# Kernel tuning notes

Measured on AMD Instinct MI355X. Metric: run time of the kernel, lower is better.

## Reference

```python
import jax, jax.numpy as jnp
import numpy as np

B, L, D = 4, 2048, 2048
NH, HD, K = 32, 64, 16
LR = 1.0
EPS = 1e-6


def ln_fwd(x, gamma, beta):
    mu = x.mean(-1, keepdims=True)
    var = jnp.var(x, axis=-1, keepdims=True)
    x_hat = (x - mu) / jnp.sqrt(var + EPS)
    return gamma * x_hat + beta


def ln_fused_l2_bwd(x, target, gamma, beta):
    # grad of 0.5*||LN(x)-target||^2 wrt x (matches LayerNormFunction.backward
    # with grad_output = LN(x) - target)
    d = x.shape[-1]
    mu = x.mean(-1, keepdims=True)
    var = jnp.var(x, axis=-1, keepdims=True)
    std = jnp.sqrt(var + EPS)
    x_hat = (x - mu) / std
    y = gamma * x_hat + beta
    g = (y - target) * gamma
    return (d * g - g.sum(-1, keepdims=True) - x_hat * (g * x_hat).sum(-1, keepdims=True)) / (d * std)


def setup_inputs() -> dict:
    key = jax.random.key(0)
    ks = jax.random.split(key, 12)
    s = 0.02
    return {
        "hidden_states": jax.random.normal(ks[0], (B, L, D), jnp.float32),
        "Wq": jax.random.normal(ks[1], (D, D), jnp.float32) * s,
        "Wk": jax.random.normal(ks[2], (D, D), jnp.float32) * s,
        "Wv": jax.random.normal(ks[3], (D, D), jnp.float32) * s,
        "Wo": jax.random.normal(ks[4], (D, D), jnp.float32) * s,
        "linear_weight": jax.random.normal(ks[5], (NH, 1, D), jnp.float32) * s,
        "linear_bias": jnp.zeros((NH, 1), jnp.float32),
        "ln_weight": jnp.ones((NH, HD), jnp.float32),
        "ln_bias": jnp.zeros((NH, HD), jnp.float32),
        "W1_init": jax.random.normal(ks[6], (NH, HD, HD), jnp.float32) * s,
        "b1_init": jnp.zeros((NH, 1, HD), jnp.float32),
    }


def reference(hidden_states, Wq, Wk, Wv, Wo, linear_weight, linear_bias,
              ln_weight, ln_bias, W1_init, b1_init):
    Bq, Lq, Dq = hidden_states.shape
    n_chunk = Lq // K

    def split(x):  # [B,L,D] -> [B,NH,n_chunk,K,HD]
        return x.reshape(Bq, n_chunk, K, NH, HD).transpose(0, 3, 1, 2, 4)

    XC = split(hidden_states @ Wq.T)
    XB = split(hidden_states @ Wk.T)
    XA = split(hidden_states @ Wv.T)

    # inner-loop learning-rate coefficient: [B,NH,n_chunk,K,1]
    X = hidden_states.reshape(Bq, n_chunk, K, Dq)
    ilr = jnp.einsum('bnkd,hd->bhnk', X, linear_weight[:, 0, :]) + linear_bias[:, 0][None, :, None, None]
    ilr_gated = jax.nn.sigmoid(ilr)[..., None]
    token_idx = 1.0 / jnp.arange(1, K + 1, dtype=hidden_states.dtype)
    coeff = (LR * token_idx).reshape(1, 1, 1, K, 1) * ilr_gated / HD

    ln_w = ln_weight.reshape(1, NH, 1, HD)
    ln_b = ln_bias.reshape(1, NH, 1, HD)
    mask = jnp.tril(jnp.ones((K, K), hidden_states.dtype))

    W1 = jnp.broadcast_to(W1_init[None], (Bq, NH, HD, HD))
    b1 = jnp.broadcast_to(b1_init[None], (Bq, NH, 1, HD))

    def step(carry, inp):
        W1, b1 = carry
        xc, xb, xa, co = inp  # [B,NH,K,HD], co: [B,NH,K,1]
        Z1 = xb @ W1 + b1
        grad = ln_fused_l2_bwd(Z1, xa - xb, ln_w, ln_b)  # [B,NH,K,HD]
        Attn = mask * jnp.einsum('bhkf,bhjf->bhkj', xc, xb)
        E = mask * co.transpose(0, 1, 3, 2)  # E[i,j] = coeff_j * (j<=i)
        b1_bar = b1 - E @ grad
        Z1_bar = xc @ W1 - (Attn * E) @ grad + b1_bar
        W1_new = W1 - jnp.einsum('bhkf,bhkg->bhfg', co * xb, grad)
        b1_new = b1 - (co * grad).sum(-2, keepdims=True)
        out = xc + ln_fwd(Z1_bar, ln_w, ln_b)
        return (W1_new, b1_new), out

    xs = (XC.transpose(2, 0, 1, 3, 4), XB.transpose(2, 0, 1, 3, 4),
          XA.transpose(2, 0, 1, 3, 4), coeff.transpose(2, 0, 1, 3, 4))
    (_, _), outs = jax.lax.scan(step, (W1, b1), xs)
    # outs: [n_chunk,B,NH,K,HD] -> [B,L,D]
    XCW = outs.transpose(1, 0, 3, 2, 4).reshape(Bq, Lq, Dq)
    return XCW @ Wo.T
```

## Files before the change

kernel.cpp:

```cpp
#include <hip/hip_runtime.h>


typedef __attribute__((ext_vector_type(4))) float float4v;
typedef __attribute__((ext_vector_type(2))) float float2v;
typedef __attribute__((ext_vector_type(8))) __bf16 bf16x8;
typedef __attribute__((ext_vector_type(4))) short short4v;
typedef __attribute__((ext_vector_type(4))) unsigned int uint4v;
typedef __attribute__((ext_vector_type(2))) unsigned int uint2v;

__device__ __forceinline__ unsigned short f2bf(float f) {
  unsigned int u = __builtin_bit_cast(unsigned int, f);
  u += 0x7FFFu + ((u >> 16) & 1u);
  return (unsigned short)(u >> 16);
}
__device__ __forceinline__ float bf2f(unsigned short s) {
  unsigned int u = ((unsigned int)s) << 16;
  return __builtin_bit_cast(float, u);
}
__device__ __forceinline__ void lds_load16(const void* g, void* l) {
  __builtin_amdgcn_global_load_lds((const __attribute__((address_space(1))) void*)g,
                                   (__attribute__((address_space(3))) void*)l, 16, 0, 0);
}

__device__ __forceinline__ void store_out(float* p, float v) { *p = v; }
__device__ __forceinline__ void store_out(unsigned short* p, float v) { *p = f2bf(v); }

template <int CTRL>
__device__ __forceinline__ float dppmov(float x) {
  return __builtin_bit_cast(
      float, __builtin_amdgcn_update_dpp(0, __builtin_bit_cast(int, x), CTRL, 0xF, 0xF, true));
}
__device__ __forceinline__ float red16(float x) {
  x += dppmov<0xB1>(x);
  x += dppmov<0x4E>(x);
  x += dppmov<0x124>(x);
  x += dppmov<0x128>(x);
  return x;
}
__device__ __forceinline__ unsigned int cvtpk_bf16(float lo, float hi) {
  unsigned int r;
  asm("v_cvt_pk_bf16_f32 %0, %1, %2" : "=v"(r) : "v"(lo), "v"(hi));
  return r;
}
__device__ __forceinline__ void bar_sync() {
  asm volatile("s_waitcnt lgkmcnt(0)" ::: "memory");
  __builtin_amdgcn_s_barrier();
  asm volatile("" ::: "memory");
}
__device__ __forceinline__ void vm_bar() {
  asm volatile("s_waitcnt vmcnt(0)" ::: "memory");
  __builtin_amdgcn_s_barrier();
  asm volatile("" ::: "memory");
}

template <typename OUT>
__global__ __launch_bounds__(256) void gemm_bt(
    const unsigned short* __restrict__ A, const unsigned short* __restrict__ B,
    OUT* __restrict__ C, int M, int N, int K) {
  __shared__ unsigned short sA[2][128 * 32];
  __shared__ unsigned short sB[2][128 * 32];
  const int tid = threadIdx.x;
  const int wave = tid >> 6;
  const int lane = tid & 63;
  const int quad = lane >> 4;
  const int l15 = lane & 15;
  const int wm = (wave >> 1) * 64;
  const int wn = (wave & 1) * 64;
  const int bm = blockIdx.y * 128;
  const int bn = blockIdx.x * 128;

  float4v acc[4][4];
#pragma unroll
  for (int i = 0; i < 4; ++i)
#pragma unroll
    for (int j = 0; j < 4; ++j) acc[i][j] = (float4v){0.f, 0.f, 0.f, 0.f};

  const int srow = tid >> 2;
  const int scol = (tid & 3) * 8;
  const unsigned short* aptr = A + (size_t)(bm + srow) * K + scol;
  const unsigned short* bptr = B + (size_t)(bn + srow) * K + scol;
  const size_t astep = (size_t)64 * K;
  const int woff = wave * 512;

  lds_load16(aptr, &sA[0][woff]);
  lds_load16(aptr + astep, &sA[0][2048 + woff]);
  lds_load16(bptr, &sB[0][woff]);
  lds_load16(bptr + astep, &sB[0][2048 + woff]);
  vm_bar();

  int cur = 0;
  for (int kt = 0; kt < K; kt += 32) {
    if (kt + 32 < K) {
      const int nxt = cur ^ 1;
      lds_load16(aptr + kt + 32, &sA[nxt][woff]);
      lds_load16(aptr + kt + 32 + astep, &sA[nxt][2048 + woff]);
      lds_load16(bptr + kt + 32, &sB[nxt][woff]);
      lds_load16(bptr + kt + 32 + astep, &sB[nxt][2048 + woff]);
    }
    bf16x8 af[4], bf[4];
#pragma unroll
    for (int i = 0; i < 4; ++i)
      af[i] = *(const bf16x8*)&sA[cur][(wm + i * 16 + l15) * 32 + quad * 8];
#pragma unroll
    for (int j = 0; j < 4; ++j)
      bf[j] = *(const bf16x8*)&sB[cur][(wn + j * 16 + l15) * 32 + quad * 8];
#pragma unroll
    for (int i = 0; i < 4; ++i)
#pragma unroll
      for (int j = 0; j < 4; ++j)
        acc[i][j] = __builtin_amdgcn_mfma_f32_16x16x32_bf16(af[i], bf[j], acc[i][j], 0, 0, 0);
    vm_bar();
    cur ^= 1;
  }

#pragma unroll
  for (int i = 0; i < 4; ++i) {
    const int row0 = bm + wm + i * 16 + quad * 4;
#pragma unroll
    for (int j = 0; j < 4; ++j) {
      const int col = bn + wn + j * 16 + l15;
#pragma unroll
      for (int r = 0; r < 4; ++r)
        store_out(&C[(size_t)(row0 + r) * N + col], acc[i][j][r]);
    }
  }
}

__global__ __launch_bounds__(256) void f32_to_bf16_k(const float* __restrict__ s,
                                                     unsigned short* __restrict__ d, int n) {
  const int i = (blockIdx.x * 256 + threadIdx.x) * 8;
  if (i >= n) return;
  const float4v a = *(const float4v*)(s + i);
  const float4v b = *(const float4v*)(s + i + 4);
  uint4v o;
  o[0] = (unsigned int)f2bf(a[0]) | ((unsigned int)f2bf(a[1]) << 16);
  o[1] = (unsigned int)f2bf(a[2]) | ((unsigned int)f2bf(a[3]) << 16);
  o[2] = (unsigned int)f2bf(b[0]) | ((unsigned int)f2bf(b[1]) << 16);
  o[3] = (unsigned int)f2bf(b[2]) | ((unsigned int)f2bf(b[3]) << 16);
  *(uint4v*)(d + i) = o;
}

__global__ __launch_bounds__(256) void coeff_k(const unsigned short* __restrict__ ilr,
                                               const float* __restrict__ lb,
                                               float* __restrict__ coeff) {
  const int gid = blockIdx.x * 256 + threadIdx.x;
  const int row = gid >> 5;
  const int h = gid & 31;
  const float v = bf2f(ilr[row * 128 + h]) + lb[h];
  const float sig = 1.0f / (1.0f + __expf(-v));
  const int b = row >> 11;
  const int pos = row & 2047;
  const int cc = pos >> 4;
  const int k = pos & 15;
  coeff[((((size_t)b * 32 + h) * 128 + cc) << 4) + k] = sig / (64.0f * (float)(k + 1));
}

__global__ __launch_bounds__(256, 1) void ttt_scan(
    const unsigned short* __restrict__ XC, const unsigned short* __restrict__ XB,
    const unsigned short* __restrict__ XA, const float* __restrict__ coeff,
    const float* __restrict__ lnw, const float* __restrict__ lnb,
    const float* __restrict__ W1i, const float* __restrict__ b1i,
    unsigned short* __restrict__ XCW) {
  const int b = blockIdx.x >> 5;
  const int h = blockIdx.x & 31;
  const int tid = threadIdx.x;
  const int wave = tid >> 6;
  const int lane = tid & 63;
  const int quad = lane >> 4;
  const int l15 = lane & 15;

  constexpr int LDW = 88;
  __shared__ __attribute__((aligned(16))) unsigned short sXC[2][16 * LDW];
  __shared__ __attribute__((aligned(16))) unsigned short sXB[2][16 * LDW];
  __shared__ __attribute__((aligned(16))) unsigned short sXA[2][16 * LDW];
  __shared__ __attribute__((aligned(16))) unsigned short sW1[64 * LDW];
  __shared__ __attribute__((aligned(16))) float sRed[3][16][8];

  const int fcol = wave * 16 + l15;
  const float gam = lnw[h * 64 + fcol];
  const float bet = lnb[h * 64 + fcol];

  float4v W1r[4];
#pragma unroll
  for (int mt = 0; mt < 4; ++mt) {
    float4v v;
#pragma unroll
    for (int r = 0; r < 4; ++r)
      v[r] = W1i[(size_t)h * 4096 + (size_t)(mt * 16 + quad * 4 + r) * 64 + fcol];
    W1r[mt] = v;
  }
  float b1v = b1i[h * 64 + fcol];

#pragma unroll
  for (int mt = 0; mt < 4; ++mt) {
    uint2v p;
    p[0] = cvtpk_bf16(W1r[mt][0], W1r[mt][1]);
    p[1] = cvtpk_bf16(W1r[mt][2], W1r[mt][3]);
    *(uint2v*)&sW1[(size_t)fcol * LDW + mt * 16 + quad * 4] = p;
  }

  const int u = tid & 127;
  const int grow = u >> 3;
  const int gcol = (u & 7) * 8;
  const size_t hdoff = (size_t)h * 64;
  const size_t browoff = (size_t)b * 2048;
  const float* cobase = coeff + (((size_t)b * 32 + h) * 128) * 16;
  const float inv64 = 1.0f / 64.0f;
  const float4v zero4 = {0.f, 0.f, 0.f, 0.f};

  uint4v pA = {0, 0, 0, 0}, pB = {0, 0, 0, 0};
  float4v pcof;
  {
    const size_t goff = (browoff + (size_t)grow) * 2048 + hdoff + gcol;
    if (tid < 128) {
      pA = *(const uint4v*)(XC + goff);
      pB = *(const uint4v*)(XA + goff);
    } else {
      pA = *(const uint4v*)(XB + goff);
    }
    pcof = *(const float4v*)(cobase + quad * 4);
  }

  for (int c = 0; c < 128; ++c) {
    const int buf = c & 1;
    if (tid < 128) {
      *(uint4v*)&sXC[buf][grow * LDW + gcol] = pA;
      *(uint4v*)&sXA[buf][grow * LDW + gcol] = pB;
    } else {
      *(uint4v*)&sXB[buf][grow * LDW + gcol] = pA;
    }
    const float4v cof = pcof;
    bar_sync();

    {
      const int cn = (c < 127) ? c + 1 : 127;
      const size_t goff = (browoff + (size_t)(cn * 16 + grow)) * 2048 + hdoff + gcol;
      if (tid < 128) {
        pA = *(const uint4v*)(XC + goff);
        pB = *(const uint4v*)(XA + goff);
      } else {
        pA = *(const uint4v*)(XB + goff);
      }
      pcof = *(const float4v*)(cobase + (size_t)cn * 16 + quad * 4);
    }

    bf16x8 xbf[2], xcf[2], w1f[2];
#pragma unroll
    for (int hh = 0; hh < 2; ++hh) {
      xbf[hh] = *(const bf16x8*)&sXB[buf][l15 * LDW + hh * 32 + quad * 8];
      xcf[hh] = *(const bf16x8*)&sXC[buf][l15 * LDW + hh * 32 + quad * 8];
      w1f[hh] = *(const bf16x8*)&sW1[(size_t)fcol * LDW + hh * 32 + quad * 8];
    }

    float4v z = __builtin_amdgcn_mfma_f32_16x16x32_bf16(xbf[0], w1f[0], zero4, 0, 0, 0);
    z = __builtin_amdgcn_mfma_f32_16x16x32_bf16(xbf[1], w1f[1], z, 0, 0, 0);
#pragma unroll
    for (int r = 0; r < 4; ++r) z[r] += b1v;

    float s1p[4], s2p[4];
#pragma unroll
    for (int r = 0; r < 4; ++r) {
      s1p[r] = red16(z[r]);
      s2p[r] = red16(z[r] * z[r]);
    }
    if (l15 == 0) {
#pragma unroll
      for (int r = 0; r < 4; ++r)
        *(float2v*)&sRed[0][quad * 4 + r][wave * 2] = (float2v){s1p[r], s2p[r]};
    }

    float4v at = __builtin_amdgcn_mfma_f32_16x16x32_bf16(xbf[0], xcf[0], zero4, 0, 0, 0);
    at = __builtin_amdgcn_mfma_f32_16x16x32_bf16(xbf[1], xcf[1], at, 0, 0, 0);

    bar_sync();

    float mu[4], rstd[4];
#pragma unroll
    for (int r = 0; r < 4; ++r) {
      const float4v v0 = *(const float4v*)&sRed[0][quad * 4 + r][0];
      const float4v v1 = *(const float4v*)&sRed[0][quad * 4 + r][4];
      const float s1 = v0[0] + v0[2] + v1[0] + v1[2];
      const float s2 = v0[1] + v0[3] + v1[1] + v1[3];
      mu[r] = s1 * inv64;
      rstd[r] = rsqrtf(s2 * inv64 - mu[r] * mu[r] + 1e-6f);
    }
    float xh[4], gg[4];
#pragma unroll
    for (int r = 0; r < 4; ++r) {
      xh[r] = (z[r] - mu[r]) * rstd[r];
      const int toff = (quad * 4 + r) * LDW + fcol;
      const float tgt = bf2f(sXA[buf][toff]) - bf2f(sXB[buf][toff]);
      gg[r] = (gam * xh[r] + bet - tgt) * gam;
    }
    float sgp[4], sgxp[4];
#pragma unroll
    for (int r = 0; r < 4; ++r) {
      sgp[r] = red16(gg[r]);
      sgxp[r] = red16(gg[r] * xh[r]);
    }
    if (l15 == 0) {
#pragma unroll
      for (int r = 0; r < 4; ++r)
        *(float2v*)&sRed[1][quad * 4 + r][wave * 2] = (float2v){sgp[r], sgxp[r]};
    }

    short4v caf[4];
#pragma unroll
    for (int mt = 0; mt < 4; ++mt)
#pragma unroll
      for (int jj = 0; jj < 4; ++jj)
        caf[mt][jj] =
            (short)f2bf(-cof[jj] * bf2f(sXB[buf][(quad * 4 + jj) * LDW + mt * 16 + l15]));
    short4v m1f;
#pragma unroll
    for (int jj = 0; jj < 4; ++jj) {
      const int k = quad * 4 + jj;
      const float e = (k <= l15) ? cof[jj] : 0.0f;
      m1f[jj] = (short)f2bf(-(at[jj] + 1.0f) * e);
    }

    bar_sync();

    float grad[4];
    short4v gradb;
#pragma unroll
    for (int r = 0; r < 4; ++r) {
      const float4v v0 = *(const float4v*)&sRed[1][quad * 4 + r][0];
      const float4v v1 = *(const float4v*)&sRed[1][quad * 4 + r][4];
      const float sg = v0[0] + v0[2] + v1[0] + v1[2];
      const float sgx = v0[1] + v0[3] + v1[1] + v1[3];
      grad[r] = (64.0f * gg[r] - sg - xh[r] * sgx) * (rstd[r] * inv64);
      gradb[r] = (short)f2bf(grad[r]);
    }

    float4v zb = __builtin_amdgcn_mfma_f32_16x16x32_bf16(xcf[0], w1f[0], zero4, 0, 0, 0);
    zb = __builtin_amdgcn_mfma_f32_16x16x32_bf16(xcf[1], w1f[1], zb, 0, 0, 0);
    zb = __builtin_amdgcn_mfma_f32_16x16x16bf16_1k(m1f, gradb, zb, 0, 0, 0);
#pragma unroll
    for (int r = 0; r < 4; ++r) zb[r] += b1v;

#pragma unroll
    for (int r = 0; r < 4; ++r) {
      s1p[r] = red16(zb[r]);
      s2p[r] = red16(zb[r] * zb[r]);
    }
    if (l15 == 0) {
#pragma unroll
      for (int r = 0; r < 4; ++r)
        *(float2v*)&sRed[2][quad * 4 + r][wave * 2] = (float2v){s1p[r], s2p[r]};
    }

    {
      float pb = cof[0] * grad[0] + cof[1] * grad[1] + cof[2] * grad[2] + cof[3] * grad[3];
      pb += __shfl_xor(pb, 16);
      pb += __shfl_xor(pb, 32);
      b1v -= pb;
    }
#pragma unroll
    for (int mt = 0; mt < 4; ++mt)
      W1r[mt] = __builtin_amdgcn_mfma_f32_16x16x16bf16_1k(caf[mt], gradb, W1r[mt], 0, 0, 0);

    bar_sync();

#pragma unroll
    for (int r = 0; r < 4; ++r) {
      const float4v v0 = *(const float4v*)&sRed[2][quad * 4 + r][0];
      const float4v v1 = *(const float4v*)&sRed[2][quad * 4 + r][4];
      const float s1 = v0[0] + v0[2] + v1[0] + v1[2];
      const float s2 = v0[1] + v0[3] + v1[1] + v1[3];
      const float mu2 = s1 * inv64;
      const float rstd2 = rsqrtf(s2 * inv64 - mu2 * mu2 + 1e-6f);
      const float xhat = (zb[r] - mu2) * rstd2;
      const float y = gam * xhat + bet;
      const float o = bf2f(sXC[buf][(quad * 4 + r) * LDW + fcol]) + y;
      XCW[(browoff + (size_t)(c * 16 + quad * 4 + r)) * 2048 + hdoff + fcol] = f2bf(o);
    }

#pragma unroll
    for (int mt = 0; mt < 4; ++mt) {
      uint2v p;
      p[0] = cvtpk_bf16(W1r[mt][0], W1r[mt][1]);
      p[1] = cvtpk_bf16(W1r[mt][2], W1r[mt][3]);
      *(uint2v*)&sW1[(size_t)fcol * LDW + mt * 16 + quad * 4] = p;
    }
  }
}

extern "C" void kernel_launch(void* const* d_in, const int* in_sizes, int n_in,
                              void* d_out, int out_size, void* d_ws, size_t ws_size,
                              hipStream_t stream) {
  const float* hs = (const float*)d_in[0];
  const float* Wq = (const float*)d_in[1];
  const float* Wk = (const float*)d_in[2];
  const float* Wv = (const float*)d_in[3];
  const float* Wo = (const float*)d_in[4];
  const float* lw = (const float*)d_in[5];
  const float* lb = (const float*)d_in[6];
  const float* lnw = (const float*)d_in[7];
  const float* lnb = (const float*)d_in[8];
  const float* W1i = (const float*)d_in[9];
  const float* b1i = (const float*)d_in[10];
  float* out = (float*)d_out;
  char* ws = (char*)d_ws;

  unsigned short* hsb = (unsigned short*)(ws);
  unsigned short* wqb = (unsigned short*)(ws + 33554432);
  unsigned short* wkb = (unsigned short*)(ws + 41943040);
  unsigned short* wvb = (unsigned short*)(ws + 50331648);
  unsigned short* wob = (unsigned short*)(ws + 58720256);
  unsigned short* lwb = (unsigned short*)(ws + 67108864);
  unsigned short* XCb = (unsigned short*)(ws + 67633152);
  unsigned short* XBb = (unsigned short*)(ws + 101187584);
  unsigned short* XAb = (unsigned short*)(ws + 134742016);
  unsigned short* ilrb = (unsigned short*)(ws + 168296448);
  float* coeff = (float*)(ws + 170393600);

  f32_to_bf16_k<<<8192, 256, 0, stream>>>(hs, hsb, 16777216);
  f32_to_bf16_k<<<2048, 256, 0, stream>>>(Wq, wqb, 4194304);
  f32_to_bf16_k<<<2048, 256, 0, stream>>>(Wk, wkb, 4194304);
  f32_to_bf16_k<<<2048, 256, 0, stream>>>(Wv, wvb, 4194304);
  f32_to_bf16_k<<<2048, 256, 0, stream>>>(Wo, wob, 4194304);
  hipMemsetAsync(lwb, 0, 524288, stream);
  f32_to_bf16_k<<<32, 256, 0, stream>>>(lw, lwb, 65536);

  dim3 blk(256);
  dim3 gbig(16, 64);
  gemm_bt<unsigned short><<<gbig, blk, 0, stream>>>(hsb, wqb, XCb, 8192, 2048, 2048);
  gemm_bt<unsigned short><<<gbig, blk, 0, stream>>>(hsb, wkb, XBb, 8192, 2048, 2048);
  gemm_bt<unsigned short><<<gbig, blk, 0, stream>>>(hsb, wvb, XAb, 8192, 2048, 2048);
  gemm_bt<unsigned short><<<dim3(1, 64), blk, 0, stream>>>(hsb, lwb, ilrb, 8192, 128, 2048);
  coeff_k<<<1024, 256, 0, stream>>>(ilrb, lb, coeff);
  ttt_scan<<<128, 256, 0, stream>>>(XCb, XBb, XAb, coeff, lnw, lnb, W1i, b1i, hsb);
  gemm_bt<float><<<gbig, blk, 0, stream>>>(hsb, wob, out, 8192, 2048, 2048);
}
```

Measured before the change: 872.0 us.

## Merge LN-backward reductions into one pass and deepen GEMM pipeline to three stages

The scan kernel now computes the LayerNorm-backward reductions (sum g, sum g*xhat) algebraically from raw moments of Z1 (sums of z, z², gamma²z, gamma²z², and target terms). All statistics are reduced in a single cross-wave exchange, which removes one block barrier per chunk. The next chunk's LDS staging is moved to the end of the iteration with a two-ahead global prefetch, so the loop needs only two barriers. The projection GEMM goes from two to three LDS stages with partial vmcnt waits, which drops the trailing barrier. The expanded moment formulas add more reductions and can lose precision when terms cancel.

```diff
diff --git a/kernel.cpp b/kernel.cpp
--- a/kernel.cpp
+++ b/kernel.cpp
@@ -47,18 +47,13 @@
   __builtin_amdgcn_s_barrier();
   asm volatile("" ::: "memory");
 }
-__device__ __forceinline__ void vm_bar() {
-  asm volatile("s_waitcnt vmcnt(0)" ::: "memory");
-  __builtin_amdgcn_s_barrier();
-  asm volatile("" ::: "memory");
-}
 
 template <typename OUT>
 __global__ __launch_bounds__(256) void gemm_bt(
     const unsigned short* __restrict__ A, const unsigned short* __restrict__ B,
     OUT* __restrict__ C, int M, int N, int K) {
-  __shared__ unsigned short sA[2][128 * 32];
-  __shared__ unsigned short sB[2][128 * 32];
+  __shared__ unsigned short sA[3][128 * 32];
+  __shared__ unsigned short sB[3][128 * 32];
   const int tid = threadIdx.x;
   const int wave = tid >> 6;
   const int lane = tid & 63;
@@ -81,37 +76,46 @@
   const unsigned short* bptr = B + (size_t)(bn + srow) * K + scol;
   const size_t astep = (size_t)64 * K;
   const int woff = wave * 512;
-
-  lds_load16(aptr, &sA[0][woff]);
-  lds_load16(aptr + astep, &sA[0][2048 + woff]);
-  lds_load16(bptr, &sB[0][woff]);
-  lds_load16(bptr + astep, &sB[0][2048 + woff]);
-  vm_bar();
-
-  int cur = 0;
-  for (int kt = 0; kt < K; kt += 32) {
-    if (kt + 32 < K) {
-      const int nxt = cur ^ 1;
-      lds_load16(aptr + kt + 32, &sA[nxt][woff]);
-      lds_load16(aptr + kt + 32 + astep, &sA[nxt][2048 + woff]);
-      lds_load16(bptr + kt + 32, &sB[nxt][woff]);
-      lds_load16(bptr + kt + 32 + astep, &sB[nxt][2048 + woff]);
-    }
+  const int nsteps = K >> 5;
+
+#define GSTAGE(t, bi)                                                   \
+  {                                                                     \
+    lds_load16(aptr + (size_t)(t) * 32, &sA[bi][woff]);                 \
+    lds_load16(aptr + (size_t)(t) * 32 + astep, &sA[bi][2048 + woff]);  \
+    lds_load16(bptr + (size_t)(t) * 32, &sB[bi][woff]);                 \
+    lds_load16(bptr + (size_t)(t) * 32 + astep, &sB[bi][2048 + woff]);  \
+  }
+
+  GSTAGE(0, 0);
+  if (nsteps > 1) GSTAGE(1, 1);
+
+  for (int i = 0; i < nsteps; ++i) {
+    if (i + 1 < nsteps) {
+      asm volatile("s_waitcnt vmcnt(4)" ::: "memory");
+    } else {
+      asm volatile("s_waitcnt vmcnt(0)" ::: "memory");
+    }
+    __builtin_amdgcn_s_barrier();
+    asm volatile("" ::: "memory");
+    if (i + 2 < nsteps) {
+      const int bi = (i + 2) % 3;
+      GSTAGE(i + 2, bi);
+    }
+    const int cb = i % 3;
     bf16x8 af[4], bf[4];
 #pragma unroll
-    for (int i = 0; i < 4; ++i)
-      af[i] = *(const bf16x8*)&sA[cur][(wm + i * 16 + l15) * 32 + quad * 8];
+    for (int ii = 0; ii < 4; ++ii)
+      af[ii] = *(const bf16x8*)&sA[cb][(wm + ii * 16 + l15) * 32 + quad * 8];
 #pragma unroll
     for (int j = 0; j < 4; ++j)
-      bf[j] = *(const bf16x8*)&sB[cur][(wn + j * 16 + l15) * 32 + quad * 8];
-#pragma unroll
-    for (int i = 0; i < 4; ++i)
+      bf[j] = *(const bf16x8*)&sB[cb][(wn + j * 16 + l15) * 32 + quad * 8];
+#pragma unroll
+    for (int ii = 0; ii < 4; ++ii)
 #pragma unroll
       for (int j = 0; j < 4; ++j)
-        acc[i][j] = __builtin_amdgcn_mfma_f32_16x16x32_bf16(af[i], bf[j], acc[i][j], 0, 0, 0);
-    vm_bar();
-    cur ^= 1;
-  }
+        acc[ii][j] = __builtin_amdgcn_mfma_f32_16x16x32_bf16(af[ii], bf[j], acc[ii][j], 0, 0, 0);
+  }
+#undef GSTAGE
 
 #pragma unroll
   for (int i = 0; i < 4; ++i) {
@@ -174,11 +178,14 @@
   __shared__ __attribute__((aligned(16))) unsigned short sXB[2][16 * LDW];
   __shared__ __attribute__((aligned(16))) unsigned short sXA[2][16 * LDW];
   __shared__ __attribute__((aligned(16))) unsigned short sW1[64 * LDW];
-  __shared__ __attribute__((aligned(16))) float sRed[3][16][8];
+  __shared__ __attribute__((aligned(16))) float sRedA[3][16][8];
+  __shared__ __attribute__((aligned(16))) float sRedB[16][8];
+  __shared__ __attribute__((aligned(16))) float sA0[4];
 
   const int fcol = wave * 16 + l15;
   const float gam = lnw[h * 64 + fcol];
   const float bet = lnb[h * 64 + fcol];
+  const float gam2 = gam * gam;
 
   float4v W1r[4];
 #pragma unroll
@@ -197,6 +204,11 @@
     p[0] = cvtpk_bf16(W1r[mt][0], W1r[mt][1]);
     p[1] = cvtpk_bf16(W1r[mt][2], W1r[mt][3]);
     *(uint2v*)&sW1[(size_t)fcol * LDW + mt * 16 + quad * 4] = p;
+  }
+
+  {
+    const float a0p = red16(gam2);
+    if (lane == 0) sA0[wave] = a0p;
   }
 
   const int u = tid & 127;
@@ -209,31 +221,162 @@
   const float4v zero4 = {0.f, 0.f, 0.f, 0.f};
 
   uint4v pA = {0, 0, 0, 0}, pB = {0, 0, 0, 0};
-  float4v pcof;
+  float4v cof, pcof;
   {
-    const size_t goff = (browoff + (size_t)grow) * 2048 + hdoff + gcol;
+    const size_t g0 = (browoff + (size_t)grow) * 2048 + hdoff + gcol;
+    uint4v a0, b0 = {0, 0, 0, 0};
     if (tid < 128) {
-      pA = *(const uint4v*)(XC + goff);
-      pB = *(const uint4v*)(XA + goff);
+      a0 = *(const uint4v*)(XC + g0);
+      b0 = *(const uint4v*)(XA + g0);
     } else {
-      pA = *(const uint4v*)(XB + goff);
-    }
-    pcof = *(const float4v*)(cobase + quad * 4);
-  }
+      a0 = *(const uint4v*)(XB + g0);
+    }
+    if (tid < 128) {
+      *(uint4v*)&sXC[0][grow * LDW + gcol] = a0;
+      *(uint4v*)&sXA[0][grow * LDW + gcol] = b0;
+    } else {
+      *(uint4v*)&sXB[0][grow * LDW + gcol] = a0;
+    }
+    cof = *(const float4v*)(cobase + quad * 4);
+    const size_t g1 = (browoff + (size_t)(16 + grow)) * 2048 + hdoff + gcol;
+    if (tid < 128) {
+      pA = *(const uint4v*)(XC + g1);
+      pB = *(const uint4v*)(XA + g1);
+    } else {
+      pA = *(const uint4v*)(XB + g1);
+    }
+    pcof = *(const float4v*)(cobase + 16 + quad * 4);
+  }
+  bar_sync();
+  const float4v a0v = *(const float4v*)sA0;
+  const float A0 = a0v[0] + a0v[1] + a0v[2] + a0v[3];
 
   for (int c = 0; c < 128; ++c) {
     const int buf = c & 1;
+
+    bf16x8 xbf[2], xcf[2], w1f[2];
+#pragma unroll
+    for (int hh = 0; hh < 2; ++hh) {
+      xbf[hh] = *(const bf16x8*)&sXB[buf][l15 * LDW + hh * 32 + quad * 8];
+      xcf[hh] = *(const bf16x8*)&sXC[buf][l15 * LDW + hh * 32 + quad * 8];
+      w1f[hh] = *(const bf16x8*)&sW1[(size_t)fcol * LDW + hh * 32 + quad * 8];
+    }
+
+    float4v at = __builtin_amdgcn_mfma_f32_16x16x32_bf16(xbf[0], xcf[0], zero4, 0, 0, 0);
+    at = __builtin_amdgcn_mfma_f32_16x16x32_bf16(xbf[1], xcf[1], at, 0, 0, 0);
+
+    float4v z = __builtin_amdgcn_mfma_f32_16x16x32_bf16(xbf[0], w1f[0], zero4, 0, 0, 0);
+    z = __builtin_amdgcn_mfma_f32_16x16x32_bf16(xbf[1], w1f[1], z, 0, 0, 0);
+#pragma unroll
+    for (int r = 0; r < 4; ++r) z[r] += b1v;
+
+    float gbt[4];
+#pragma unroll
+    for (int r = 0; r < 4; ++r) {
+      const int toff = (quad * 4 + r) * LDW + fcol;
+      const float tgt = bf2f(sXA[buf][toff]) - bf2f(sXB[buf][toff]);
+      gbt[r] = gam * (bet - tgt);
+    }
+#pragma unroll
+    for (int r = 0; r < 4; ++r) {
+      const float zz = z[r];
+      const float s1 = red16(zz);
+      const float s2 = red16(zz * zz);
+      const float a1 = red16(gam2 * zz);
+      const float a2 = red16(gam2 * zz * zz);
+      const float c0 = red16(gbt[r]);
+      const float c1 = red16(gbt[r] * zz);
+      if (l15 == 0) {
+        const int t = quad * 4 + r;
+        *(float2v*)&sRedA[0][t][wave * 2] = (float2v){s1, s2};
+        *(float2v*)&sRedA[1][t][wave * 2] = (float2v){a1, a2};
+        *(float2v*)&sRedA[2][t][wave * 2] = (float2v){c0, c1};
+      }
+    }
+
+    short4v m1f;
+#pragma unroll
+    for (int jj = 0; jj < 4; ++jj) {
+      const int k = quad * 4 + jj;
+      const float e = (k <= l15) ? cof[jj] : 0.0f;
+      m1f[jj] = (short)f2bf(-(at[jj] + 1.0f) * e);
+    }
+    short4v caf[4];
+#pragma unroll
+    for (int mt = 0; mt < 4; ++mt)
+#pragma unroll
+      for (int jj = 0; jj < 4; ++jj)
+        caf[mt][jj] =
+            (short)f2bf(-cof[jj] * bf2f(sXB[buf][(quad * 4 + jj) * LDW + mt * 16 + l15]));
+
+    bar_sync();
+
+    float xh[4], grad[4];
+    short4v gradb;
+#pragma unroll
+    for (int r = 0; r < 4; ++r) {
+      const int t = quad * 4 + r;
+      const float4v p0 = *(const float4v*)&sRedA[0][t][0];
+      const float4v p0b = *(const float4v*)&sRedA[0][t][4];
+      const float4v p1 = *(const float4v*)&sRedA[1][t][0];
+      const float4v p1b = *(const float4v*)&sRedA[1][t][4];
+      const float4v p2 = *(const float4v*)&sRedA[2][t][0];
+      const float4v p2b = *(const float4v*)&sRedA[2][t][4];
+      const float s1 = p0[0] + p0[2] + p0b[0] + p0b[2];
+      const float s2 = p0[1] + p0[3] + p0b[1] + p0b[3];
+      const float a1 = p1[0] + p1[2] + p1b[0] + p1b[2];
+      const float a2 = p1[1] + p1[3] + p1b[1] + p1b[3];
+      const float c0 = p2[0] + p2[2] + p2b[0] + p2b[2];
+      const float c1 = p2[1] + p2[3] + p2b[1] + p2b[3];
+      const float mu = s1 * inv64;
+      const float rstd = rsqrtf(s2 * inv64 - mu * mu + 1e-6f);
+      const float sg = rstd * (a1 - mu * A0) + c0;
+      const float sgx =
+          rstd * rstd * (a2 - 2.0f * mu * a1 + mu * mu * A0) + rstd * (c1 - mu * c0);
+      xh[r] = (z[r] - mu) * rstd;
+      const float gg = gam2 * xh[r] + gbt[r];
+      grad[r] = (64.0f * gg - sg - xh[r] * sgx) * (rstd * inv64);
+      gradb[r] = (short)f2bf(grad[r]);
+    }
+
+    float4v zb = __builtin_amdgcn_mfma_f32_16x16x32_bf16(xcf[0], w1f[0], zero4, 0, 0, 0);
+    zb = __builtin_amdgcn_mfma_f32_16x16x32_bf16(xcf[1], w1f[1], zb, 0, 0, 0);
+    zb = __builtin_amdgcn_mfma_f32_16x16x16bf16_1k(m1f, gradb, zb, 0, 0, 0);
+#pragma unroll
+    for (int r = 0; r < 4; ++r) zb[r] += b1v;
+
+#pragma unroll
+    for (int r = 0; r < 4; ++r) {
+      const float s1p = red16(zb[r]);
+      const float s2p = red16(zb[r] * zb[r]);
+      if (l15 == 0) *(float2v*)&sRedB[quad * 4 + r][wave * 2] = (float2v){s1p, s2p};
+    }
+
+#pragma unroll
+    for (int mt = 0; mt < 4; ++mt)
+      W1r[mt] = __builtin_amdgcn_mfma_f32_16x16x16bf16_1k(caf[mt], gradb, W1r[mt], 0, 0, 0);
+    {
+      float pb = cof[0] * grad[0] + cof[1] * grad[1] + cof[2] * grad[2] + cof[3] * grad[3];
+      pb += __shfl_xor(pb, 16);
+      pb += __shfl_xor(pb, 32);
+      b1v -= pb;
+    }
+#pragma unroll
+    for (int mt = 0; mt < 4; ++mt) {
+      uint2v p;
+      p[0] = cvtpk_bf16(W1r[mt][0], W1r[mt][1]);
+      p[1] = cvtpk_bf16(W1r[mt][2], W1r[mt][3]);
+      *(uint2v*)&sW1[(size_t)fcol * LDW + mt * 16 + quad * 4] = p;
+    }
+
     if (tid < 128) {
-      *(uint4v*)&sXC[buf][grow * LDW + gcol] = pA;
-      *(uint4v*)&sXA[buf][grow * LDW + gcol] = pB;
+      *(uint4v*)&sXC[buf ^ 1][grow * LDW + gcol] = pA;
+      *(uint4v*)&sXA[buf ^ 1][grow * LDW + gcol] = pB;
     } else {
-      *(uint4v*)&sXB[buf][grow * LDW + gcol] = pA;
-    }
-    const float4v cof = pcof;
-    bar_sync();
-
+      *(uint4v*)&sXB[buf ^ 1][grow * LDW + gcol] = pA;
+    }
     {
-      const int cn = (c < 127) ? c + 1 : 127;
+      const int cn = (c < 126) ? c + 2 : 127;
       const size_t goff = (browoff + (size_t)(cn * 16 + grow)) * 2048 + hdoff + gcol;
       if (tid < 128) {
         pA = *(const uint4v*)(XC + goff);
@@ -241,147 +384,25 @@
       } else {
         pA = *(const uint4v*)(XB + goff);
       }
+      cof = pcof;
       pcof = *(const float4v*)(cobase + (size_t)cn * 16 + quad * 4);
     }
 
-    bf16x8 xbf[2], xcf[2], w1f[2];
-#pragma unroll
-    for (int hh = 0; hh < 2; ++hh) {
-      xbf[hh] = *(const bf16x8*)&sXB[buf][l15 * LDW + hh * 32 + quad * 8];
-      xcf[hh] = *(const bf16x8*)&sXC[buf][l15 * LDW + hh * 32 + quad * 8];
-      w1f[hh] = *(const bf16x8*)&sW1[(size_t)fcol * LDW + hh * 32 + quad * 8];
-    }
-
-    float4v z = __builtin_amdgcn_mfma_f32_16x16x32_bf16(xbf[0], w1f[0], zero4, 0, 0, 0);
-    z = __builtin_amdgcn_mfma_f32_16x16x32_bf16(xbf[1], w1f[1], z, 0, 0, 0);
-#pragma unroll
-    for (int r = 0; r < 4; ++r) z[r] += b1v;
-
-    float s1p[4], s2p[4];
+    bar_sync();
+
 #pragma unroll
     for (int r = 0; r < 4; ++r) {
-      s1p[r] = red16(z[r]);
-      s2p[r] = red16(z[r] * z[r]);
-    }
-    if (l15 == 0) {
-#pragma unroll
-      for (int r = 0; r < 4; ++r)
-        *(float2v*)&sRed[0][quad * 4 + r][wave * 2] = (float2v){s1p[r], s2p[r]};
-    }
-
-    float4v at = __builtin_amdgcn_mfma_f32_16x16x32_bf16(xbf[0], xcf[0], zero4, 0, 0, 0);
-    at = __builtin_amdgcn_mfma_f32_16x16x32_bf16(xbf[1], xcf[1], at, 0, 0, 0);
-
-    bar_sync();
-
-    float mu[4], rstd[4];
-#pragma unroll
-    for (int r = 0; r < 4; ++r) {
-      const float4v v0 = *(const float4v*)&sRed[0][quad * 4 + r][0];
-      const float4v v1 = *(const float4v*)&sRed[0][quad * 4 + r][4];
-      const float s1 = v0[0] + v0[2] + v1[0] + v1[2];
-      const float s2 = v0[1] + v0[3] + v1[1] + v1[3];
-      mu[r] = s1 * inv64;
-      rstd[r] = rsqrtf(s2 * inv64 - mu[r] * mu[r] + 1e-6f);
-    }
-    float xh[4], gg[4];
-#pragma unroll
-    for (int r = 0; r < 4; ++r) {
-      xh[r] = (z[r] - mu[r]) * rstd[r];
-      const int toff = (quad * 4 + r) * LDW + fcol;
-      const float tgt = bf2f(sXA[buf][toff]) - bf2f(sXB[buf][toff]);
-      gg[r] = (gam * xh[r] + bet - tgt) * gam;
-    }
-    float sgp[4], sgxp[4];
-#pragma unroll
-    for (int r = 0; r < 4; ++r) {
-      sgp[r] = red16(gg[r]);
-      sgxp[r] = red16(gg[r] * xh[r]);
-    }
-    if (l15 == 0) {
-#pragma unroll
-      for (int r = 0; r < 4; ++r)
-        *(float2v*)&sRed[1][quad * 4 + r][wave * 2] = (float2v){sgp[r], sgxp[r]};
-    }
-
-    short4v caf[4];
-#pragma unroll
-    for (int mt = 0; mt < 4; ++mt)
-#pragma unroll
-      for (int jj = 0; jj < 4; ++jj)
-        caf[mt][jj] =
-            (short)f2bf(-cof[jj] * bf2f(sXB[buf][(quad * 4 + jj) * LDW + mt * 16 + l15]));
-    short4v m1f;
-#pragma unroll
-    for (int jj = 0; jj < 4; ++jj) {
-      const int k = quad * 4 + jj;
-      const float e = (k <= l15) ? cof[jj] : 0.0f;
-      m1f[jj] = (short)f2bf(-(at[jj] + 1.0f) * e);
-    }
-
-    bar_sync();
-
-    float grad[4];
-    short4v gradb;
-#pragma unroll
-    for (int r = 0; r < 4; ++r) {
-      const float4v v0 = *(const float4v*)&sRed[1][quad * 4 + r][0];
-      const float4v v1 = *(const float4v*)&sRed[1][quad * 4 + r][4];
-      const float sg = v0[0] + v0[2] + v1[0] + v1[2];
-      const float sgx = v0[1] + v0[3] + v1[1] + v1[3];
-      grad[r] = (64.0f * gg[r] - sg - xh[r] * sgx) * (rstd[r] * inv64);
-      gradb[r] = (short)f2bf(grad[r]);
-    }
-
-    float4v zb = __builtin_amdgcn_mfma_f32_16x16x32_bf16(xcf[0], w1f[0], zero4, 0, 0, 0);
-    zb = __builtin_amdgcn_mfma_f32_16x16x32_bf16(xcf[1], w1f[1], zb, 0, 0, 0);
-    zb = __builtin_amdgcn_mfma_f32_16x16x16bf16_1k(m1f, gradb, zb, 0, 0, 0);
-#pragma unroll
-    for (int r = 0; r < 4; ++r) zb[r] += b1v;
-
-#pragma unroll
-    for (int r = 0; r < 4; ++r) {
-      s1p[r] = red16(zb[r]);
-      s2p[r] = red16(zb[r] * zb[r]);
-    }
-    if (l15 == 0) {
-#pragma unroll
-      for (int r = 0; r < 4; ++r)
-        *(float2v*)&sRed[2][quad * 4 + r][wave * 2] = (float2v){s1p[r], s2p[r]};
-    }
-
-    {
-      float pb = cof[0] * grad[0] + cof[1] * grad[1] + cof[2] * grad[2] + cof[3] * grad[3];
-      pb += __shfl_xor(pb, 16);
-      pb += __shfl_xor(pb, 32);
-      b1v -= pb;
-    }
-#pragma unroll
-    for (int mt = 0; mt < 4; ++mt)
-      W1r[mt] = __builtin_amdgcn_mfma_f32_16x16x16bf16_1k(caf[mt], gradb, W1r[mt], 0, 0, 0);
-
-    bar_sync();
-
-#pragma unroll
-    for (int r = 0; r < 4; ++r) {
-      const float4v v0 = *(const float4v*)&sRed[2][quad * 4 + r][0];
-      const float4v v1 = *(const float4v*)&sRed[2][quad * 4 + r][4];
-      const float s1 = v0[0] + v0[2] + v1[0] + v1[2];
-      const float s2 = v0[1] + v0[3] + v1[1] + v1[3];
+      const int t = quad * 4 + r;
+      const float4v q0 = *(const float4v*)&sRedB[t][0];
+      const float4v q1 = *(const float4v*)&sRedB[t][4];
+      const float s1 = q0[0] + q0[2] + q1[0] + q1[2];
+      const float s2 = q0[1] + q0[3] + q1[1] + q1[3];
       const float mu2 = s1 * inv64;
       const float rstd2 = rsqrtf(s2 * inv64 - mu2 * mu2 + 1e-6f);
       const float xhat = (zb[r] - mu2) * rstd2;
       const float y = gam * xhat + bet;
-      const float o = bf2f(sXC[buf][(quad * 4 + r) * LDW + fcol]) + y;
-      XCW[(browoff + (size_t)(c * 16 + quad * 4 + r)) * 2048 + hdoff + fcol] = f2bf(o);
-    }
-
-#pragma unroll
-    for (int mt = 0; mt < 4; ++mt) {
-      uint2v p;
-      p[0] = cvtpk_bf16(W1r[mt][0], W1r[mt][1]);
-      p[1] = cvtpk_bf16(W1r[mt][2], W1r[mt][3]);
-      *(uint2v*)&sW1[(size_t)fcol * LDW + mt * 16 + quad * 4] = p;
+      const float o = bf2f(sXC[buf][t * LDW + fcol]) + y;
+      XCW[(browoff + (size_t)(c * 16 + t)) * 2048 + hdoff + fcol] = f2bf(o);
     }
   }
 }
```

Result: slower. 923.7 us (+5.9%).

## Replace projection GEMMs with 256x256-tile triple-buffered swizzled GEMM kernel

Applied to the files above, without the earlier changes.

Adds a new GEMM kernel that uses 256x256 output tiles with 8 waves, a three-stage LDS ring filled by async global-to-LDS loads, XOR-swizzled LDS chunks, an XCD-aware block remap, and raised wave priority around the MFMA clusters. The Q/K/V projections and the output projection now use it, which aims for more data reuse per tile and less exposed load latency than the 128x128 double-buffered kernel. The costs are more registers and LDS per block and only 256 blocks per GEMM, which may leave some CUs underused.

```diff
diff --git a/kernel.cpp b/kernel.cpp
--- a/kernel.cpp
+++ b/kernel.cpp
@@ -47,10 +47,118 @@
   __builtin_amdgcn_s_barrier();
   asm volatile("" ::: "memory");
 }
-__device__ __forceinline__ void vm_bar() {
-  asm volatile("s_waitcnt vmcnt(0)" ::: "memory");
-  __builtin_amdgcn_s_barrier();
-  asm volatile("" ::: "memory");
+
+template <typename OUT>
+__global__ __launch_bounds__(512, 2) void gemm256(
+    const unsigned short* __restrict__ A, const unsigned short* __restrict__ B,
+    OUT* __restrict__ C, int M, int N, int K) {
+  __shared__ unsigned short sA[3][256 * 32];
+  __shared__ unsigned short sB[3][256 * 32];
+  const int tid = threadIdx.x;
+  const int wave = tid >> 6;
+  const int lane = tid & 63;
+  const int quad = lane >> 4;
+  const int l15 = lane & 15;
+  const int wm = (wave >> 2) * 128;
+  const int wn = (wave & 3) * 64;
+
+  const int nwg = gridDim.x;
+  const int cpx = nwg >> 3;
+  const int o = blockIdx.x;
+  const int wgid = (o & 7) * cpx + (o >> 3);
+  const int nbx = N >> 8;
+  const int bm = (wgid / nbx) * 256;
+  const int bn = (wgid % nbx) * 256;
+
+  float4v acc[8][4];
+#pragma unroll
+  for (int i = 0; i < 8; ++i)
+#pragma unroll
+    for (int j = 0; j < 4; ++j) acc[i][j] = (float4v){0.f, 0.f, 0.f, 0.f};
+
+  const int srow = tid >> 2;
+  const int schunk = (tid & 3) ^ (srow & 3);
+  const unsigned short* aS = A + (size_t)(bm + srow) * K + schunk * 8;
+  const unsigned short* bS = B + (size_t)(bn + srow) * K + schunk * 8;
+  const size_t hstep = (size_t)128 * K;
+  const int ldsw = wave * 512;
+
+#define STAGE_A(t, bi)                                                \
+  {                                                                   \
+    lds_load16(aS + (size_t)(t) * 32, &sA[bi][ldsw]);                 \
+    lds_load16(aS + (size_t)(t) * 32 + hstep, &sA[bi][4096 + ldsw]);  \
+  }
+#define STAGE_B(t, bi)                                                \
+  {                                                                   \
+    lds_load16(bS + (size_t)(t) * 32, &sB[bi][ldsw]);                 \
+    lds_load16(bS + (size_t)(t) * 32 + hstep, &sB[bi][4096 + ldsw]);  \
+  }
+
+  const int NT = K >> 5;
+  STAGE_A(0, 0);
+  STAGE_B(0, 0);
+  STAGE_A(1, 1);
+  STAGE_B(1, 1);
+
+  const int sw = (quad ^ (l15 & 3)) * 8;
+
+  for (int T = 0; T < NT; ++T) {
+    const int cur = T % 3;
+    const int dst = (T + 2) % 3;
+    if (T + 1 < NT) {
+      asm volatile("s_waitcnt vmcnt(4)" ::: "memory");
+    } else {
+      asm volatile("s_waitcnt vmcnt(0)" ::: "memory");
+    }
+    __builtin_amdgcn_s_barrier();
+    asm volatile("" ::: "memory");
+
+    if (T + 2 < NT) {
+      STAGE_A(T + 2, dst);
+      STAGE_B(T + 2, dst);
+    }
+
+    bf16x8 bfr[4], afr[4];
+#pragma unroll
+    for (int nt = 0; nt < 4; ++nt)
+      bfr[nt] = *(const bf16x8*)&sB[cur][(wn + nt * 16 + l15) * 32 + sw];
+#pragma unroll
+    for (int mt = 0; mt < 4; ++mt)
+      afr[mt] = *(const bf16x8*)&sA[cur][(wm + mt * 16 + l15) * 32 + sw];
+    __builtin_amdgcn_s_setprio(1);
+#pragma unroll
+    for (int mt = 0; mt < 4; ++mt)
+#pragma unroll
+      for (int nt = 0; nt < 4; ++nt)
+        acc[mt][nt] = __builtin_amdgcn_mfma_f32_16x16x32_bf16(afr[mt], bfr[nt], acc[mt][nt], 0, 0, 0);
+    __builtin_amdgcn_s_setprio(0);
+
+#pragma unroll
+    for (int mt = 0; mt < 4; ++mt)
+      afr[mt] = *(const bf16x8*)&sA[cur][(wm + 64 + mt * 16 + l15) * 32 + sw];
+    __builtin_amdgcn_s_setprio(1);
+#pragma unroll
+    for (int mt = 0; mt < 4; ++mt)
+#pragma unroll
+      for (int nt = 0; nt < 4; ++nt)
+        acc[4 + mt][nt] = __builtin_amdgcn_mfma_f32_16x16x32_bf16(afr[mt], bfr[nt], acc[4 + mt][nt], 0, 0, 0);
+    __builtin_amdgcn_s_setprio(0);
+    asm volatile("" ::: "memory");
+  }
+#undef STAGE_A
+#undef STAGE_B
+
+#pragma unroll
+  for (int mt = 0; mt < 8; ++mt) {
+    const int row0 = bm + wm + mt * 16 + quad * 4;
+#pragma unroll
+    for (int nt = 0; nt < 4; ++nt) {
+      const int col = bn + wn + nt * 16 + l15;
+#pragma unroll
+      for (int r = 0; r < 4; ++r)
+        store_out(&C[(size_t)(row0 + r) * N + col], acc[mt][nt][r]);
+    }
+  }
 }
 
 template <typename OUT>
@@ -86,7 +194,9 @@
   lds_load16(aptr + astep, &sA[0][2048 + woff]);
   lds_load16(bptr, &sB[0][woff]);
   lds_load16(bptr + astep, &sB[0][2048 + woff]);
-  vm_bar();
+  asm volatile("s_waitcnt vmcnt(0)" ::: "memory");
+  __builtin_amdgcn_s_barrier();
+  asm volatile("" ::: "memory");
 
   int cur = 0;
   for (int kt = 0; kt < K; kt += 32) {
@@ -109,7 +219,9 @@
 #pragma unroll
       for (int j = 0; j < 4; ++j)
         acc[i][j] = __builtin_amdgcn_mfma_f32_16x16x32_bf16(af[i], bf[j], acc[i][j], 0, 0, 0);
-    vm_bar();
+    asm volatile("s_waitcnt vmcnt(0)" ::: "memory");
+    __builtin_amdgcn_s_barrier();
+    asm volatile("" ::: "memory");
     cur ^= 1;
   }
 
@@ -423,13 +535,11 @@
   hipMemsetAsync(lwb, 0, 524288, stream);
   f32_to_bf16_k<<<32, 256, 0, stream>>>(lw, lwb, 65536);
 
-  dim3 blk(256);
-  dim3 gbig(16, 64);
-  gemm_bt<unsigned short><<<gbig, blk, 0, stream>>>(hsb, wqb, XCb, 8192, 2048, 2048);
-  gemm_bt<unsigned short><<<gbig, blk, 0, stream>>>(hsb, wkb, XBb, 8192, 2048, 2048);
-  gemm_bt<unsigned short><<<gbig, blk, 0, stream>>>(hsb, wvb, XAb, 8192, 2048, 2048);
-  gemm_bt<unsigned short><<<dim3(1, 64), blk, 0, stream>>>(hsb, lwb, ilrb, 8192, 128, 2048);
+  gemm256<unsigned short><<<256, 512, 0, stream>>>(hsb, wqb, XCb, 8192, 2048, 2048);
+  gemm256<unsigned short><<<256, 512, 0, stream>>>(hsb, wkb, XBb, 8192, 2048, 2048);
+  gemm256<unsigned short><<<256, 512, 0, stream>>>(hsb, wvb, XAb, 8192, 2048, 2048);
+  gemm_bt<unsigned short><<<dim3(1, 64), dim3(256), 0, stream>>>(hsb, lwb, ilrb, 8192, 128, 2048);
   coeff_k<<<1024, 256, 0, stream>>>(ilrb, lb, coeff);
   ttt_scan<<<128, 256, 0, stream>>>(XCb, XBb, XAb, coeff, lnw, lnb, W1i, b1i, hsb);
-  gemm_bt<float><<<gbig, blk, 0, stream>>>(hsb, wob, out, 8192, 2048, 2048);
-}
+  gemm256<float><<<256, 512, 0, stream>>>(hsb, wob, out, 8192, 2048, 2048);
+}
```

Measured after the change: 857.8 us. About the same (-1.6%).
